# Kernel optimization log

Measured on AMD Instinct MI355X. Metric: run time of the kernel, lower is better.

The kernel has to match this reference:

```python
import jax, jax.numpy as jnp
import numpy as np

BATCH, SEQ, D_MODEL, D_STATE = 8, 4096, 128, 128


def setup_inputs() -> dict:
    key = jax.random.key(0)
    ks = jax.random.split(key, 6)
    x = jax.random.normal(ks[0], (BATCH, SEQ, D_MODEL), jnp.float32)
    # Stable (negative) eigenvalues so A_discrete = exp(dt*Lambda) < 1 and powers don't overflow.
    Lam = -(jax.random.uniform(ks[1], (D_STATE,), jnp.float32) * 2.0 + 0.1)
    B = jax.random.normal(ks[2], (D_STATE, D_MODEL), jnp.float32) / np.sqrt(D_STATE)
    C = jax.random.normal(ks[3], (D_MODEL, D_STATE), jnp.float32) / np.sqrt(D_STATE)
    Dv = jax.random.normal(ks[4], (D_MODEL,), jnp.float32)
    log_dt = (jax.random.uniform(ks[5], (D_MODEL,), jnp.float32)
              * (np.log(0.001) - np.log(0.1)) + np.log(0.1)).astype(jnp.float32)
    return {"x": x, "Lam": Lam, "B": B, "C": C, "Dv": Dv, "log_dt": log_dt}


def _s4_forward(x, Lam, B, C, Dv, log_dt):
    # x: (batch, L, M) with transposed=False
    _, L, M = x.shape
    dt = jnp.exp(log_dt)                                    # (M,)
    rate = dt[:, None] * Lam[None, :]                       # (M, N) = log(A_discrete)
    ell = jnp.arange(L, dtype=x.dtype)                      # (L,)
    # powers[m, s, l] = A_discrete[m, s] ** l  (closed form of the sequential cumprod)
    powers = jnp.exp(rate[:, :, None] * ell[None, None, :])  # (M, N, L)
    # Original: einsum('ds,msl->dsl', B, powers) sums over m, giving B[d,s]*Psum[s,l];
    # then einsum('md,dsl->ml', C, .) contracts d and s -> kernel = C @ B @ Psum.
    Psum = powers.sum(axis=0)                               # (N, L)
    kernel = C @ (B @ Psum)                                 # (M, L)
    xt = jnp.transpose(x, (0, 2, 1))                        # (B, M, L)
    n = 2 * L  # zero-padded linear convolution via FFT
    y_fft = jnp.fft.rfft(xt, n=n) * jnp.fft.rfft(kernel, n=n)[None]
    y = jnp.fft.irfft(y_fft, n=n)[..., :L]                  # (B, M, L)
    y = y + Dv[None, :, None] * xt                          # skip connection D*u
    return jnp.transpose(y, (0, 2, 1))                      # (B, L, M)


def reference(x, Lam, B, C, Dv, log_dt):
    return _s4_forward(x, Lam, B, C, Dv, log_dt)
```

## Files before the change

kernel.cpp:

```cpp
#include <hip/hip_runtime.h>
#include <math.h>

#define BATCH 8
#define SEQ   4096
#define DM    128
#define DS    128
#define N2    4096
#define NT    256
#define NTP   256

__device__ __forceinline__ float2 cmulf(float2 a, float2 b) {
    return make_float2(a.x * b.x - a.y * b.y, a.x * b.y + a.y * b.x);
}
__device__ __forceinline__ float2 caddf(float2 a, float2 b) { return make_float2(a.x + b.x, a.y + b.y); }
__device__ __forceinline__ float2 csubf(float2 a, float2 b) { return make_float2(a.x - b.x, a.y - b.y); }
__device__ __forceinline__ float2 conjf2(float2 a) { return make_float2(a.x, -a.y); }
__device__ __forceinline__ float2 cisf(float t) { float s, c; __sincosf(t, &s, &c); return make_float2(c, s); }

__device__ __forceinline__ int nibrev(int k) { return ((k & 15) << 8) | (k & 0xF0) | (k >> 8); }
__device__ __forceinline__ int physi(int a) { return a ^ ((a >> 4) & 15); }

__device__ __forceinline__ void dft16_fwd(const float2 x[16], float2 Xh[16]) {
    const float2 W[10] = { {1.f,0.f},
        {0.92387953f,-0.38268343f},{0.70710678f,-0.70710678f},{0.38268343f,-0.92387953f},
        {0.f,-1.f},{-0.38268343f,-0.92387953f},{-0.70710678f,-0.70710678f},
        {-0.92387953f,-0.38268343f},{-1.f,0.f},{-0.92387953f,0.38268343f} };
    float2 y[16];
#pragma unroll
    for (int j = 0; j < 4; ++j) {
        float2 a0 = x[j], a1 = x[j+4], a2 = x[j+8], a3 = x[j+12];
        float2 t0 = caddf(a0,a2), t1 = csubf(a0,a2);
        float2 t2 = caddf(a1,a3), t3 = csubf(a1,a3);
        float2 b1 = make_float2(t1.x + t3.y, t1.y - t3.x);
        float2 b3 = make_float2(t1.x - t3.y, t1.y + t3.x);
        y[j]    = caddf(t0,t2);
        y[j+4]  = cmulf(b1, W[j]);
        y[j+8]  = cmulf(csubf(t0,t2), W[2*j]);
        y[j+12] = cmulf(b3, W[3*j]);
    }
#pragma unroll
    for (int g = 0; g < 4; ++g) {
        float2 a0 = y[4*g], a1 = y[4*g+1], a2 = y[4*g+2], a3 = y[4*g+3];
        float2 t0 = caddf(a0,a2), t1 = csubf(a0,a2);
        float2 t2 = caddf(a1,a3), t3 = csubf(a1,a3);
        Xh[4*g]   = caddf(t0,t2);
        Xh[4*g+1] = make_float2(t1.x + t3.y, t1.y - t3.x);
        Xh[4*g+2] = csubf(t0,t2);
        Xh[4*g+3] = make_float2(t1.x - t3.y, t1.y + t3.x);
    }
}
__device__ __forceinline__ void dft16_inv(const float2 x[16], float2 Xh[16]) {
    const float2 W[10] = { {1.f,0.f},
        {0.92387953f,0.38268343f},{0.70710678f,0.70710678f},{0.38268343f,0.92387953f},
        {0.f,1.f},{-0.38268343f,0.92387953f},{-0.70710678f,0.70710678f},
        {-0.92387953f,0.38268343f},{-1.f,0.f},{-0.92387953f,-0.38268343f} };
    float2 y[16];
#pragma unroll
    for (int j = 0; j < 4; ++j) {
        float2 a0 = x[j], a1 = x[j+4], a2 = x[j+8], a3 = x[j+12];
        float2 t0 = caddf(a0,a2), t1 = csubf(a0,a2);
        float2 t2 = caddf(a1,a3), t3 = csubf(a1,a3);
        float2 b1 = make_float2(t1.x - t3.y, t1.y + t3.x);
        float2 b3 = make_float2(t1.x + t3.y, t1.y - t3.x);
        y[j]    = caddf(t0,t2);
        y[j+4]  = cmulf(b1, W[j]);
        y[j+8]  = cmulf(csubf(t0,t2), W[2*j]);
        y[j+12] = cmulf(b3, W[3*j]);
    }
#pragma unroll
    for (int g = 0; g < 4; ++g) {
        float2 a0 = y[4*g], a1 = y[4*g+1], a2 = y[4*g+2], a3 = y[4*g+3];
        float2 t0 = caddf(a0,a2), t1 = csubf(a0,a2);
        float2 t2 = caddf(a1,a3), t3 = csubf(a1,a3);
        Xh[4*g]   = caddf(t0,t2);
        Xh[4*g+1] = make_float2(t1.x - t3.y, t1.y + t3.x);
        Xh[4*g+2] = csubf(t0,t2);
        Xh[4*g+3] = make_float2(t1.x + t3.y, t1.y - t3.x);
    }
}


template<int Q>
__device__ __forceinline__ void stage_fwd(float2* z, int t) {
    float2 x[16], Xh[16];
    int adr[16];
    if (Q == 16) {
        int j = t & 15, top = t >> 4;
#pragma unroll
        for (int r = 0; r < 16; ++r) adr[r] = (top << 8) + (r << 4) + (j ^ r);
    } else {
        int j4 = t & 15;
#pragma unroll
        for (int r = 0; r < 16; ++r) adr[r] = (t << 4) + (j4 ^ r);
    }
#pragma unroll
    for (int r = 0; r < 16; ++r) x[r] = z[adr[r]];
    dft16_fwd(x, Xh);
    if (Q > 1) {
        int j = t & (Q - 1);
        float2 w1 = cisf(-(float)M_PI / (8.0f * (float)Q) * (float)j);
        float2 w = make_float2(1.f, 0.f);
#pragma unroll
        for (int k = 0; k < 16; ++k) {
            int sk = ((k & 3) << 2) | (k >> 2);
            z[adr[k]] = cmulf(Xh[sk], w);
            w = cmulf(w, w1);
        }
    } else {
#pragma unroll
        for (int k = 0; k < 16; ++k) {
            int sk = ((k & 3) << 2) | (k >> 2);
            z[adr[k]] = Xh[sk];
        }
    }
}

template<int Q>
__device__ __forceinline__ void stage_inv(float2* z, int t) {
    float2 x[16], Xh[16];
    int adr[16];
    if (Q == 16) {
        int j = t & 15, top = t >> 4;
#pragma unroll
        for (int r = 0; r < 16; ++r) adr[r] = (top << 8) + (r << 4) + (j ^ r);
    } else {
        int j4 = t & 15;
#pragma unroll
        for (int r = 0; r < 16; ++r) adr[r] = (t << 4) + (j4 ^ r);
    }
    if (Q > 1) {
        int j = t & (Q - 1);
        float2 w1 = cisf((float)M_PI / (8.0f * (float)Q) * (float)j);
        float2 w = make_float2(1.f, 0.f);
#pragma unroll
        for (int k = 0; k < 16; ++k) {
            x[k] = cmulf(z[adr[k]], w);
            w = cmulf(w, w1);
        }
    } else {
#pragma unroll
        for (int k = 0; k < 16; ++k) x[k] = z[adr[k]];
    }
    dft16_inv(x, Xh);
#pragma unroll
    for (int r = 0; r < 16; ++r) {
        int sr = ((r & 3) << 2) | (r >> 2);
        z[adr[r]] = Xh[sr];
    }
}

__device__ __forceinline__ void fwd_first(float2* z, const float2* __restrict__ vrow, int t) {
    float2 x[16], Xh[16];
#pragma unroll
    for (int r = 0; r < 8; ++r) x[r] = vrow[t + (r << 8)];
#pragma unroll
    for (int r = 8; r < 16; ++r) x[r] = make_float2(0.f, 0.f);
    dft16_fwd(x, Xh);
    int b0 = t ^ ((t >> 4) & 15);
    float2 w1 = cisf(-(float)M_PI / 2048.0f * (float)t);
    float2 w = make_float2(1.f, 0.f);
#pragma unroll
    for (int k = 0; k < 16; ++k) {
        int sk = ((k & 3) << 2) | (k >> 2);
        z[b0 + (k << 8)] = cmulf(Xh[sk], w);
        w = cmulf(w, w1);
    }
}

__device__ __forceinline__ void inv_last_store(const float2* z, float2* __restrict__ xrow,
                                               int t, float dv) {
    float2 x[16], Xh[16];
    int b0 = t ^ ((t >> 4) & 15);
    float2 w1 = cisf((float)M_PI / 2048.0f * (float)t);
    float2 w = make_float2(1.f, 0.f);
#pragma unroll
    for (int k = 0; k < 16; ++k) {
        x[k] = cmulf(z[b0 + (k << 8)], w);
        w = cmulf(w, w1);
    }
    dft16_inv(x, Xh);
    const float invN = 1.0f / 4096.0f;
#pragma unroll
    for (int r = 0; r < 8; ++r) {
        int sr = ((r & 3) << 2) | (r >> 2);
        float2 res = Xh[sr];
        float2 xv = xrow[t + (r << 8)];
        xrow[t + (r << 8)] = make_float2(res.x * invN + dv * xv.x, res.y * invN + dv * xv.y);
    }
}

__device__ __forceinline__ void pq_one(float2 Kk, float2 Kkp, float thk,
                                       float2 fap, float2 fbp,
                                       float2* P, float2* Q) {
    float2 e  = cisf(-thk);
    float2 fa = make_float2(0.5f * (1.f + e.y), -0.5f * e.x);
    float2 fb = make_float2(0.5f * (1.f - e.y),  0.5f * e.x);
    float2 ak = cmulf(Kk, fa), bk = cmulf(Kk, fb);
    float2 apv = cmulf(Kkp, fap), bpv = cmulf(Kkp, fbp);
    float2 g = make_float2(0.5f * (1.f + e.y), 0.5f * e.x);
    float2 h = make_float2(0.5f * (1.f - e.y), -0.5f * e.x);
    *P = caddf(cmulf(g, ak), cmulf(h, conjf2(bpv)));
    *Q = caddf(cmulf(g, bk), cmulf(h, conjf2(apv)));
}
__device__ __forceinline__ void pq_pair(float2 Kk, float2 Kkp, float thk, float thkp,
                                        float2* Pk, float2* Qk, float2* Pkp, float2* Qkp) {
    float2 e  = cisf(-thk);
    float2 ep = cisf(-thkp);
    float2 fa  = make_float2(0.5f * (1.f + e.y),  -0.5f * e.x);
    float2 fb  = make_float2(0.5f * (1.f - e.y),   0.5f * e.x);
    float2 fap = make_float2(0.5f * (1.f + ep.y), -0.5f * ep.x);
    float2 fbp = make_float2(0.5f * (1.f - ep.y),  0.5f * ep.x);
    pq_one(Kk,  Kkp, thk,  fap, fbp, Pk,  Qk);
    pq_one(Kkp, Kk,  thkp, fa,  fb,  Pkp, Qkp);
}


__global__ void prep_G(const float* __restrict__ Cm, const float* __restrict__ Bm,
                       float* __restrict__ GT) {
    int gid = blockIdx.x * blockDim.x + threadIdx.x;
    int m = gid >> 7, j = gid & 127;
    float acc = 0.f;
    for (int i = 0; i < DS; ++i) acc += Cm[m * DS + i] * Bm[i * DM + j];
    GT[j * DM + m] = acc;
}

__global__ void prep_psum2(const float* __restrict__ Lam, const float* __restrict__ logdt,
                           float* __restrict__ Psum) {
    __shared__ float E[DM];
    int s = blockIdx.x >> 1, half = blockIdx.x & 1;
    int t = threadIdx.x;
    if (t < DM) E[t] = __expf(logdt[t]) * Lam[s];
    __syncthreads();
    int l0 = t + 2048 * half;
    float acc[8] = {0.f,0.f,0.f,0.f,0.f,0.f,0.f,0.f};
    for (int m = 0; m < DM; ++m) {
        float e = E[m];
        float w = __expf(e * (float)l0);
        float r = __expf(e * 256.0f);
#pragma unroll
        for (int i = 0; i < 8; ++i) { acc[i] += w; w *= r; }
    }
#pragma unroll
    for (int i = 0; i < 8; ++i) Psum[s * SEQ + l0 + 256 * i] = acc[i];
}

__global__ void prep_K2(const float* __restrict__ GT, const float* __restrict__ Psum,
                        float* __restrict__ K) {
    __shared__ float4 PT[DS][4];
    int l0 = blockIdx.x * 16;
    int t = threadIdx.x;
    for (int idx = t; idx < 512; idx += NTP) {
        int s = idx >> 2, q = idx & 3;
        PT[s][q] = ((const float4*)(Psum + s * SEQ + l0))[q];
    }
    __syncthreads();
    int m = t & 127, half = t >> 7;
    float acc[8] = {0.f,0.f,0.f,0.f,0.f,0.f,0.f,0.f};
    for (int s = 0; s < DS; ++s) {
        float g = GT[s * DM + m];
        float4 p0 = PT[s][half * 2], p1 = PT[s][half * 2 + 1];
        acc[0] += g * p0.x; acc[1] += g * p0.y; acc[2] += g * p0.z; acc[3] += g * p0.w;
        acc[4] += g * p1.x; acc[5] += g * p1.y; acc[6] += g * p1.z; acc[7] += g * p1.w;
    }
    float4* kp = (float4*)(K + (size_t)m * SEQ + l0 + half * 8);
    kp[0] = make_float4(acc[0], acc[1], acc[2], acc[3]);
    kp[1] = make_float4(acc[4], acc[5], acc[6], acc[7]);
}

__global__ void __launch_bounds__(NT, 4) fftK_PQ(const float* __restrict__ K,
                                                 float4* __restrict__ PQ) {
    __shared__ __align__(16) float2 z[N2];
    int t = threadIdx.x, m = blockIdx.x;
    const float2* krow = (const float2*)(K + (size_t)m * SEQ);

    fwd_first(z, krow, t);  __syncthreads();
    stage_fwd<16>(z, t);    __syncthreads();
    stage_fwd<1>(z, t);     __syncthreads();

    float4* dst = PQ + (size_t)m * 4096;
#pragma unroll
    for (int c = 0; c < 8; ++c) {
        int idx2 = (((c << 8) | t)) << 1;
        int pos = (t << 4) | c;
        float2 Pk, Qk, Pkp, Qkp;
        if (pos == 0) {
            float2 v0 = z[0];
            float2 v2 = z[8];
            float2 Ku0    = make_float2(v0.x + v0.y, 0.f);
            float2 Ku4096 = make_float2(v0.x - v0.y, 0.f);
            float2 Ku2048 = conjf2(v2);
            float2 Pd, Qd;
            pq_pair(Ku0, Ku4096, 0.f, (float)M_PI, &Pk, &Qk, &Pd, &Qd);
            float th2 = 0.5f * (float)M_PI;
            pq_pair(Ku2048, Ku2048, th2, th2, &Pkp, &Qkp, &Pd, &Qd);
        } else {
            int k  = nibrev(pos);
            int kp = 4096 - k;
            float2 va = z[physi(pos)];
            float2 vb = z[physi(nibrev(kp))];
            float thk  = (float)M_PI * (float)k / 4096.0f;
            float thkp = (float)M_PI - thk;
            float2 e  = cisf(-thk);
            float2 cb = conjf2(vb);
            float2 s  = caddf(va, cb), d = csubf(va, cb);
            float2 pr = cmulf(e, d);
            float2 Kuk = make_float2(0.5f * (s.x + pr.y), 0.5f * (s.y - pr.x));
            float2 ep = make_float2(-e.x, e.y);
            float2 ca = conjf2(va);
            float2 s2 = caddf(vb, ca), d2 = csubf(vb, ca);
            float2 p2 = cmulf(ep, d2);
            float2 Kukp = make_float2(0.5f * (s2.x + p2.y), 0.5f * (s2.y - p2.x));
            pq_pair(Kuk, Kukp, thk, thkp, &Pk, &Qk, &Pkp, &Qkp);
        }
        dst[idx2]     = make_float4(Pk.x, Pk.y, Qk.x, Qk.y);
        dst[idx2 + 1] = make_float4(Pkp.x, Pkp.y, Qkp.x, Qkp.y);
    }
}

__global__ void __launch_bounds__(NT, 4) conv16(float* __restrict__ xt,
                                                const float4* __restrict__ PQ,
                                                const float* __restrict__ Dv) {
    __shared__ __align__(16) float2 z[N2];
    int t = threadIdx.x;
    int m = blockIdx.x & (DM - 1);
    int b = blockIdx.x >> 7;
    float2* xrow = (float2*)(xt + (((size_t)b * DM + m) << 12));

    fwd_first(z, xrow, t);  __syncthreads();
    stage_fwd<16>(z, t);    __syncthreads();
    stage_fwd<1>(z, t);     __syncthreads();

    {
        const float4* pq = PQ + (size_t)m * 4096;
#pragma unroll
        for (int c = 0; c < 8; ++c) {
            int idx2 = (((c << 8) | t)) << 1;
            int pos = (t << 4) | c;
            float4 lo = pq[idx2];
            float4 hi = pq[idx2 + 1];
            if (pos == 0) {
                float2 v0 = z[0];
                z[0] = caddf(cmulf(make_float2(lo.x, lo.y), v0),
                             cmulf(make_float2(lo.z, lo.w), conjf2(v0)));
                float2 v2 = z[8];
                z[8] = caddf(cmulf(make_float2(hi.x, hi.y), v2),
                             cmulf(make_float2(hi.z, hi.w), conjf2(v2)));
            } else {
                int k  = nibrev(pos);
                int i  = physi(pos);
                int ip = physi(nibrev(4096 - k));
                float2 va = z[i], vb = z[ip];
                z[i]  = caddf(cmulf(make_float2(lo.x, lo.y), va),
                              cmulf(make_float2(lo.z, lo.w), conjf2(vb)));
                z[ip] = caddf(cmulf(make_float2(hi.x, hi.y), vb),
                              cmulf(make_float2(hi.z, hi.w), conjf2(va)));
            }
        }
    }
    __syncthreads();

    stage_inv<1>(z, t);     __syncthreads();
    stage_inv<16>(z, t);    __syncthreads();
    inv_last_store(z, xrow, t, Dv[m]);
}

__global__ void transpose_xin(const float* __restrict__ x, float* __restrict__ xt) {
    __shared__ float tile[32][33];
    int b = blockIdx.z;
    int l0 = blockIdx.x * 32, m0 = blockIdx.y * 32;
    int t = threadIdx.x;
    int lr = t >> 3, mc4 = (t & 7) * 4;
    float4 v = *(const float4*)&x[(size_t)b * SEQ * DM + (size_t)(l0 + lr) * DM + m0 + mc4];
    tile[lr][mc4 + 0] = v.x; tile[lr][mc4 + 1] = v.y;
    tile[lr][mc4 + 2] = v.z; tile[lr][mc4 + 3] = v.w;
    __syncthreads();
    int mr = t >> 3, lc4 = (t & 7) * 4;
    float4 o = make_float4(tile[lc4 + 0][mr], tile[lc4 + 1][mr],
                           tile[lc4 + 2][mr], tile[lc4 + 3][mr]);
    *(float4*)&xt[(size_t)b * DM * SEQ + (size_t)(m0 + mr) * SEQ + l0 + lc4] = o;
}

__global__ void transpose_yout(const float* __restrict__ yt, float* __restrict__ out) {
    __shared__ float tile[32][33];
    int b = blockIdx.z;
    int l0 = blockIdx.x * 32, m0 = blockIdx.y * 32;
    int t = threadIdx.x;
    int mr = t >> 3, lc4 = (t & 7) * 4;
    float4 v = *(const float4*)&yt[(size_t)b * DM * SEQ + (size_t)(m0 + mr) * SEQ + l0 + lc4];
    tile[mr][lc4 + 0] = v.x; tile[mr][lc4 + 1] = v.y;
    tile[mr][lc4 + 2] = v.z; tile[mr][lc4 + 3] = v.w;
    __syncthreads();
    int lr = t >> 3, mc4 = (t & 7) * 4;
    float4 o = make_float4(tile[mc4 + 0][lr], tile[mc4 + 1][lr],
                           tile[mc4 + 2][lr], tile[mc4 + 3][lr]);
    *(float4*)&out[(size_t)b * SEQ * DM + (size_t)(l0 + lr) * DM + m0 + mc4] = o;
}

extern "C" void kernel_launch(void* const* d_in, const int* in_sizes, int n_in,
                              void* d_out, int out_size, void* d_ws, size_t ws_size,
                              hipStream_t stream) {
    const float* x     = (const float*)d_in[0];
    const float* Lam   = (const float*)d_in[1];
    const float* Bm    = (const float*)d_in[2];
    const float* Cm    = (const float*)d_in[3];
    const float* Dv    = (const float*)d_in[4];
    const float* logdt = (const float*)d_in[5];
    float* out = (float*)d_out;

    float*  ws   = (float*)d_ws;
    float*  xt   = ws;
    float4* PQ   = (float4*)(ws + 4194304);
    float*  K    = ws + 4194304 + 2097152;
    float*  Psum = K + 524288;
    float*  GT   = Psum + 524288;

    hipLaunchKernelGGL(prep_G,         dim3(64),         dim3(NTP),  0, stream, Cm, Bm, GT);
    hipLaunchKernelGGL(prep_psum2,     dim3(256),        dim3(NTP),  0, stream, Lam, logdt, Psum);
    hipLaunchKernelGGL(prep_K2,        dim3(256),        dim3(NTP),  0, stream, GT, Psum, K);
    hipLaunchKernelGGL(fftK_PQ,        dim3(128),        dim3(NT),   0, stream, K, PQ);
    hipLaunchKernelGGL(transpose_xin,  dim3(128, 4, 8),  dim3(NT),   0, stream, x, xt);
    hipLaunchKernelGGL(conv16,         dim3(1024),       dim3(NT),   0, stream, xt, PQ, Dv);
    hipLaunchKernelGGL(transpose_yout, dim3(128, 4, 8),  dim3(NT),   0, stream, xt, out);
}
```

Before: 134.8 us.

## Process two batch rows per FFT convolution block to reuse spectral filter loads

The convolution kernel now handles two batch elements for the same channel in one block, with two shared-memory FFT buffers. Each PQ filter coefficient load is shared across both rows, and per-thread twiddle computation and address setup are amortized over two independent FFTs, which also adds instruction-level parallelism. In exchange the grid halves to 512 blocks, shared memory per block doubles, register pressure roughly doubles, and launch bounds drop to 2 blocks per SM, which lowers occupancy.

```diff
diff --git a/kernel.cpp b/kernel.cpp
--- a/kernel.cpp
+++ b/kernel.cpp
@@ -115,40 +115,6 @@
     }
 }
 
-template<int Q>
-__device__ __forceinline__ void stage_inv(float2* z, int t) {
-    float2 x[16], Xh[16];
-    int adr[16];
-    if (Q == 16) {
-        int j = t & 15, top = t >> 4;
-#pragma unroll
-        for (int r = 0; r < 16; ++r) adr[r] = (top << 8) + (r << 4) + (j ^ r);
-    } else {
-        int j4 = t & 15;
-#pragma unroll
-        for (int r = 0; r < 16; ++r) adr[r] = (t << 4) + (j4 ^ r);
-    }
-    if (Q > 1) {
-        int j = t & (Q - 1);
-        float2 w1 = cisf((float)M_PI / (8.0f * (float)Q) * (float)j);
-        float2 w = make_float2(1.f, 0.f);
-#pragma unroll
-        for (int k = 0; k < 16; ++k) {
-            x[k] = cmulf(z[adr[k]], w);
-            w = cmulf(w, w1);
-        }
-    } else {
-#pragma unroll
-        for (int k = 0; k < 16; ++k) x[k] = z[adr[k]];
-    }
-    dft16_inv(x, Xh);
-#pragma unroll
-    for (int r = 0; r < 16; ++r) {
-        int sr = ((r & 3) << 2) | (r >> 2);
-        z[adr[r]] = Xh[sr];
-    }
-}
-
 __device__ __forceinline__ void fwd_first(float2* z, const float2* __restrict__ vrow, int t) {
     float2 x[16], Xh[16];
 #pragma unroll
@@ -167,25 +133,127 @@
     }
 }
 
-__device__ __forceinline__ void inv_last_store(const float2* z, float2* __restrict__ xrow,
-                                               int t, float dv) {
-    float2 x[16], Xh[16];
+
+template<int Q>
+__device__ __forceinline__ void stage_fwd2(float2* z0, float2* z1, int t) {
+    float2 x0[16], X0[16], x1[16], X1[16];
+    int adr[16];
+    if (Q == 16) {
+        int j = t & 15, top = t >> 4;
+#pragma unroll
+        for (int r = 0; r < 16; ++r) adr[r] = (top << 8) + (r << 4) + (j ^ r);
+    } else {
+        int j4 = t & 15;
+#pragma unroll
+        for (int r = 0; r < 16; ++r) adr[r] = (t << 4) + (j4 ^ r);
+    }
+#pragma unroll
+    for (int r = 0; r < 16; ++r) { x0[r] = z0[adr[r]]; x1[r] = z1[adr[r]]; }
+    dft16_fwd(x0, X0);
+    dft16_fwd(x1, X1);
+    if (Q > 1) {
+        int j = t & (Q - 1);
+        float2 w1 = cisf(-(float)M_PI / (8.0f * (float)Q) * (float)j);
+        float2 w = make_float2(1.f, 0.f);
+#pragma unroll
+        for (int k = 0; k < 16; ++k) {
+            int sk = ((k & 3) << 2) | (k >> 2);
+            z0[adr[k]] = cmulf(X0[sk], w);
+            z1[adr[k]] = cmulf(X1[sk], w);
+            w = cmulf(w, w1);
+        }
+    } else {
+#pragma unroll
+        for (int k = 0; k < 16; ++k) {
+            int sk = ((k & 3) << 2) | (k >> 2);
+            z0[adr[k]] = X0[sk];
+            z1[adr[k]] = X1[sk];
+        }
+    }
+}
+
+template<int Q>
+__device__ __forceinline__ void stage_inv2(float2* z0, float2* z1, int t) {
+    float2 x0[16], X0[16], x1[16], X1[16];
+    int adr[16];
+    if (Q == 16) {
+        int j = t & 15, top = t >> 4;
+#pragma unroll
+        for (int r = 0; r < 16; ++r) adr[r] = (top << 8) + (r << 4) + (j ^ r);
+    } else {
+        int j4 = t & 15;
+#pragma unroll
+        for (int r = 0; r < 16; ++r) adr[r] = (t << 4) + (j4 ^ r);
+    }
+    if (Q > 1) {
+        int j = t & (Q - 1);
+        float2 w1 = cisf((float)M_PI / (8.0f * (float)Q) * (float)j);
+        float2 w = make_float2(1.f, 0.f);
+#pragma unroll
+        for (int k = 0; k < 16; ++k) {
+            x0[k] = cmulf(z0[adr[k]], w);
+            x1[k] = cmulf(z1[adr[k]], w);
+            w = cmulf(w, w1);
+        }
+    } else {
+#pragma unroll
+        for (int k = 0; k < 16; ++k) { x0[k] = z0[adr[k]]; x1[k] = z1[adr[k]]; }
+    }
+    dft16_inv(x0, X0);
+    dft16_inv(x1, X1);
+#pragma unroll
+    for (int r = 0; r < 16; ++r) {
+        int sr = ((r & 3) << 2) | (r >> 2);
+        z0[adr[r]] = X0[sr];
+        z1[adr[r]] = X1[sr];
+    }
+}
+
+__device__ __forceinline__ void fwd_first2(float2* z0, float2* z1,
+                                           const float2* __restrict__ v0,
+                                           const float2* __restrict__ v1, int t) {
+    float2 x0[16], X0[16], x1[16], X1[16];
+#pragma unroll
+    for (int r = 0; r < 8; ++r) { x0[r] = v0[t + (r << 8)]; x1[r] = v1[t + (r << 8)]; }
+#pragma unroll
+    for (int r = 8; r < 16; ++r) { x0[r] = make_float2(0.f,0.f); x1[r] = make_float2(0.f,0.f); }
+    dft16_fwd(x0, X0);
+    dft16_fwd(x1, X1);
+    int b0 = t ^ ((t >> 4) & 15);
+    float2 w1 = cisf(-(float)M_PI / 2048.0f * (float)t);
+    float2 w = make_float2(1.f, 0.f);
+#pragma unroll
+    for (int k = 0; k < 16; ++k) {
+        int sk = ((k & 3) << 2) | (k >> 2);
+        z0[b0 + (k << 8)] = cmulf(X0[sk], w);
+        z1[b0 + (k << 8)] = cmulf(X1[sk], w);
+        w = cmulf(w, w1);
+    }
+}
+
+__device__ __forceinline__ void inv_last_store2(const float2* z0, const float2* z1,
+                                                float2* __restrict__ v0, float2* __restrict__ v1,
+                                                int t, float dv) {
+    float2 x0[16], X0[16], x1[16], X1[16];
     int b0 = t ^ ((t >> 4) & 15);
     float2 w1 = cisf((float)M_PI / 2048.0f * (float)t);
     float2 w = make_float2(1.f, 0.f);
 #pragma unroll
     for (int k = 0; k < 16; ++k) {
-        x[k] = cmulf(z[b0 + (k << 8)], w);
+        x0[k] = cmulf(z0[b0 + (k << 8)], w);
+        x1[k] = cmulf(z1[b0 + (k << 8)], w);
         w = cmulf(w, w1);
     }
-    dft16_inv(x, Xh);
+    dft16_inv(x0, X0);
+    dft16_inv(x1, X1);
     const float invN = 1.0f / 4096.0f;
 #pragma unroll
     for (int r = 0; r < 8; ++r) {
         int sr = ((r & 3) << 2) | (r >> 2);
-        float2 res = Xh[sr];
-        float2 xv = xrow[t + (r << 8)];
-        xrow[t + (r << 8)] = make_float2(res.x * invN + dv * xv.x, res.y * invN + dv * xv.y);
+        float2 xv0 = v0[t + (r << 8)];
+        float2 xv1 = v1[t + (r << 8)];
+        v0[t + (r << 8)] = make_float2(X0[sr].x * invN + dv * xv0.x, X0[sr].y * invN + dv * xv0.y);
+        v1[t + (r << 8)] = make_float2(X1[sr].x * invN + dv * xv1.x, X1[sr].y * invN + dv * xv1.y);
     }
 }
 
@@ -317,18 +385,20 @@
     }
 }
 
-__global__ void __launch_bounds__(NT, 4) conv16(float* __restrict__ xt,
-                                                const float4* __restrict__ PQ,
-                                                const float* __restrict__ Dv) {
-    __shared__ __align__(16) float2 z[N2];
+__global__ void __launch_bounds__(NT, 2) conv2(float* __restrict__ xt,
+                                               const float4* __restrict__ PQ,
+                                               const float* __restrict__ Dv) {
+    __shared__ __align__(16) float2 z0[N2];
+    __shared__ __align__(16) float2 z1[N2];
     int t = threadIdx.x;
-    int m = blockIdx.x & (DM - 1);
-    int b = blockIdx.x >> 7;
-    float2* xrow = (float2*)(xt + (((size_t)b * DM + m) << 12));
-
-    fwd_first(z, xrow, t);  __syncthreads();
-    stage_fwd<16>(z, t);    __syncthreads();
-    stage_fwd<1>(z, t);     __syncthreads();
+    int m  = blockIdx.x & (DM - 1);
+    int pr = blockIdx.x >> 7;
+    float2* xrow0 = (float2*)(xt + (((size_t)(2 * pr) * DM + m) << 12));
+    float2* xrow1 = (float2*)(xt + (((size_t)(2 * pr + 1) * DM + m) << 12));
+
+    fwd_first2(z0, z1, xrow0, xrow1, t);  __syncthreads();
+    stage_fwd2<16>(z0, z1, t);            __syncthreads();
+    stage_fwd2<1>(z0, z1, t);             __syncthreads();
 
     {
         const float4* pq = PQ + (size_t)m * 4096;
@@ -338,30 +408,33 @@
             int pos = (t << 4) | c;
             float4 lo = pq[idx2];
             float4 hi = pq[idx2 + 1];
+            float2 Plo = make_float2(lo.x, lo.y), Qlo = make_float2(lo.z, lo.w);
+            float2 Phi = make_float2(hi.x, hi.y), Qhi = make_float2(hi.z, hi.w);
             if (pos == 0) {
-                float2 v0 = z[0];
-                z[0] = caddf(cmulf(make_float2(lo.x, lo.y), v0),
-                             cmulf(make_float2(lo.z, lo.w), conjf2(v0)));
-                float2 v2 = z[8];
-                z[8] = caddf(cmulf(make_float2(hi.x, hi.y), v2),
-                             cmulf(make_float2(hi.z, hi.w), conjf2(v2)));
+                float2 a0 = z0[0], a1 = z1[0];
+                z0[0] = caddf(cmulf(Plo, a0), cmulf(Qlo, conjf2(a0)));
+                z1[0] = caddf(cmulf(Plo, a1), cmulf(Qlo, conjf2(a1)));
+                float2 b0 = z0[8], b1 = z1[8];
+                z0[8] = caddf(cmulf(Phi, b0), cmulf(Qhi, conjf2(b0)));
+                z1[8] = caddf(cmulf(Phi, b1), cmulf(Qhi, conjf2(b1)));
             } else {
                 int k  = nibrev(pos);
                 int i  = physi(pos);
                 int ip = physi(nibrev(4096 - k));
-                float2 va = z[i], vb = z[ip];
-                z[i]  = caddf(cmulf(make_float2(lo.x, lo.y), va),
-                              cmulf(make_float2(lo.z, lo.w), conjf2(vb)));
-                z[ip] = caddf(cmulf(make_float2(hi.x, hi.y), vb),
-                              cmulf(make_float2(hi.z, hi.w), conjf2(va)));
+                float2 va0 = z0[i], vb0 = z0[ip];
+                float2 va1 = z1[i], vb1 = z1[ip];
+                z0[i]  = caddf(cmulf(Plo, va0), cmulf(Qlo, conjf2(vb0)));
+                z0[ip] = caddf(cmulf(Phi, vb0), cmulf(Qhi, conjf2(va0)));
+                z1[i]  = caddf(cmulf(Plo, va1), cmulf(Qlo, conjf2(vb1)));
+                z1[ip] = caddf(cmulf(Phi, vb1), cmulf(Qhi, conjf2(va1)));
             }
         }
     }
     __syncthreads();
 
-    stage_inv<1>(z, t);     __syncthreads();
-    stage_inv<16>(z, t);    __syncthreads();
-    inv_last_store(z, xrow, t, Dv[m]);
+    stage_inv2<1>(z0, z1, t);             __syncthreads();
+    stage_inv2<16>(z0, z1, t);            __syncthreads();
+    inv_last_store2(z0, z1, xrow0, xrow1, t, Dv[m]);
 }
 
 __global__ void transpose_xin(const float* __restrict__ x, float* __restrict__ xt) {
@@ -419,6 +492,6 @@
     hipLaunchKernelGGL(prep_K2,        dim3(256),        dim3(NTP),  0, stream, GT, Psum, K);
     hipLaunchKernelGGL(fftK_PQ,        dim3(128),        dim3(NT),   0, stream, K, PQ);
     hipLaunchKernelGGL(transpose_xin,  dim3(128, 4, 8),  dim3(NT),   0, stream, x, xt);
-    hipLaunchKernelGGL(conv16,         dim3(1024),       dim3(NT),   0, stream, xt, PQ, Dv);
+    hipLaunchKernelGGL(conv2,          dim3(512),        dim3(NT),   0, stream, xt, PQ, Dv);
     hipLaunchKernelGGL(transpose_yout, dim3(128, 4, 8),  dim3(NT),   0, stream, xt, out);
 }
```

Result: no change. 136.8 us (+1.4%).

## Fuse spectral multiply into first inverse FFT stage and merge prep kernels

Applied to the files above, without the earlier changes.

The conv kernel now computes the pointwise spectral product into registers per thread and feeds it directly into a radix-16 inverse DFT. This replaces a separate shared-memory write pass, a barrier and the stage_inv<1> pass. The PQ coefficient table is re-laid out (pqslot) so each thread's 16 coefficients load with coalesced access. The prep_G and prep_psum kernels are merged into one launch to cut launch overhead. Each thread now reads 32 shared values with a less regular pattern for the partner index, and the fused block keeps more registers live.

```diff
diff --git a/kernel.cpp b/kernel.cpp
--- a/kernel.cpp
+++ b/kernel.cpp
@@ -19,6 +19,7 @@
 
 __device__ __forceinline__ int nibrev(int k) { return ((k & 15) << 8) | (k & 0xF0) | (k >> 8); }
 __device__ __forceinline__ int physi(int a) { return a ^ ((a >> 4) & 15); }
+__device__ __forceinline__ int pqslot(int p) { return ((p & 15) << 8) | (p >> 4); }
 
 __device__ __forceinline__ void dft16_fwd(const float2 x[16], float2 Xh[16]) {
     const float2 W[10] = { {1.f,0.f},
@@ -214,34 +215,33 @@
     pq_one(Kkp, Kk,  thkp, fa,  fb,  Pkp, Qkp);
 }
 
-
-__global__ void prep_G(const float* __restrict__ Cm, const float* __restrict__ Bm,
-                       float* __restrict__ GT) {
-    int gid = blockIdx.x * blockDim.x + threadIdx.x;
-    int m = gid >> 7, j = gid & 127;
-    float acc = 0.f;
-    for (int i = 0; i < DS; ++i) acc += Cm[m * DS + i] * Bm[i * DM + j];
-    GT[j * DM + m] = acc;
-}
-
-__global__ void prep_psum2(const float* __restrict__ Lam, const float* __restrict__ logdt,
-                           float* __restrict__ Psum) {
-    __shared__ float E[DM];
-    int s = blockIdx.x >> 1, half = blockIdx.x & 1;
-    int t = threadIdx.x;
-    if (t < DM) E[t] = __expf(logdt[t]) * Lam[s];
-    __syncthreads();
-    int l0 = t + 2048 * half;
-    float acc[8] = {0.f,0.f,0.f,0.f,0.f,0.f,0.f,0.f};
-    for (int m = 0; m < DM; ++m) {
-        float e = E[m];
-        float w = __expf(e * (float)l0);
-        float r = __expf(e * 256.0f);
-#pragma unroll
-        for (int i = 0; i < 8; ++i) { acc[i] += w; w *= r; }
-    }
-#pragma unroll
-    for (int i = 0; i < 8; ++i) Psum[s * SEQ + l0 + 256 * i] = acc[i];
+__global__ void __launch_bounds__(NTP) prep_GP(
+    const float* __restrict__ Lam, const float* __restrict__ logdt, float* __restrict__ Psum,
+    const float* __restrict__ Cm, const float* __restrict__ Bm, float* __restrict__ GT) {
+    int bid = blockIdx.x, t = threadIdx.x;
+    if (bid < 256) {
+        __shared__ float E[DM];
+        int s = bid >> 1, half = bid & 1;
+        if (t < DM) E[t] = __expf(logdt[t]) * Lam[s];
+        __syncthreads();
+        int l0 = t + 2048 * half;
+        float acc[8] = {0.f,0.f,0.f,0.f,0.f,0.f,0.f,0.f};
+        for (int m = 0; m < DM; ++m) {
+            float e = E[m];
+            float w = __expf(e * (float)l0);
+            float r = __expf(e * 256.0f);
+#pragma unroll
+            for (int i = 0; i < 8; ++i) { acc[i] += w; w *= r; }
+        }
+#pragma unroll
+        for (int i = 0; i < 8; ++i) Psum[s * SEQ + l0 + 256 * i] = acc[i];
+    } else {
+        int gid = (bid - 256) * NTP + t;
+        int m = gid >> 7, j = gid & 127;
+        float acc = 0.f;
+        for (int i = 0; i < DS; ++i) acc += Cm[m * DS + i] * Bm[i * DM + j];
+        GT[j * DM + m] = acc;
+    }
 }
 
 __global__ void prep_K2(const float* __restrict__ GT, const float* __restrict__ Psum,
@@ -280,7 +280,6 @@
     float4* dst = PQ + (size_t)m * 4096;
 #pragma unroll
     for (int c = 0; c < 8; ++c) {
-        int idx2 = (((c << 8) | t)) << 1;
         int pos = (t << 4) | c;
         float2 Pk, Qk, Pkp, Qkp;
         if (pos == 0) {
@@ -293,11 +292,14 @@
             pq_pair(Ku0, Ku4096, 0.f, (float)M_PI, &Pk, &Qk, &Pd, &Qd);
             float th2 = 0.5f * (float)M_PI;
             pq_pair(Ku2048, Ku2048, th2, th2, &Pkp, &Qkp, &Pd, &Qd);
+            dst[pqslot(0)] = make_float4(Pk.x, Pk.y, Qk.x, Qk.y);
+            dst[pqslot(8)] = make_float4(Pkp.x, Pkp.y, Qkp.x, Qkp.y);
         } else {
             int k  = nibrev(pos);
             int kp = 4096 - k;
+            int ppos = nibrev(kp);
             float2 va = z[physi(pos)];
-            float2 vb = z[physi(nibrev(kp))];
+            float2 vb = z[physi(ppos)];
             float thk  = (float)M_PI * (float)k / 4096.0f;
             float thkp = (float)M_PI - thk;
             float2 e  = cisf(-thk);
@@ -311,9 +313,9 @@
             float2 p2 = cmulf(ep, d2);
             float2 Kukp = make_float2(0.5f * (s2.x + p2.y), 0.5f * (s2.y - p2.x));
             pq_pair(Kuk, Kukp, thk, thkp, &Pk, &Qk, &Pkp, &Qkp);
-        }
-        dst[idx2]     = make_float4(Pk.x, Pk.y, Qk.x, Qk.y);
-        dst[idx2 + 1] = make_float4(Pkp.x, Pkp.y, Qkp.x, Qkp.y);
+            dst[pqslot(pos)]  = make_float4(Pk.x, Pk.y, Qk.x, Qk.y);
+            dst[pqslot(ppos)] = make_float4(Pkp.x, Pkp.y, Qkp.x, Qkp.y);
+        }
     }
 }
 
@@ -330,36 +332,35 @@
     stage_fwd<16>(z, t);    __syncthreads();
     stage_fwd<1>(z, t);     __syncthreads();
 
+    float2 x[16];
     {
         const float4* pq = PQ + (size_t)m * 4096;
-#pragma unroll
-        for (int c = 0; c < 8; ++c) {
-            int idx2 = (((c << 8) | t)) << 1;
-            int pos = (t << 4) | c;
-            float4 lo = pq[idx2];
-            float4 hi = pq[idx2 + 1];
-            if (pos == 0) {
-                float2 v0 = z[0];
-                z[0] = caddf(cmulf(make_float2(lo.x, lo.y), v0),
-                             cmulf(make_float2(lo.z, lo.w), conjf2(v0)));
-                float2 v2 = z[8];
-                z[8] = caddf(cmulf(make_float2(hi.x, hi.y), v2),
-                             cmulf(make_float2(hi.z, hi.w), conjf2(v2)));
-            } else {
-                int k  = nibrev(pos);
-                int i  = physi(pos);
-                int ip = physi(nibrev(4096 - k));
-                float2 va = z[i], vb = z[ip];
-                z[i]  = caddf(cmulf(make_float2(lo.x, lo.y), va),
-                              cmulf(make_float2(lo.z, lo.w), conjf2(vb)));
-                z[ip] = caddf(cmulf(make_float2(hi.x, hi.y), vb),
-                              cmulf(make_float2(hi.z, hi.w), conjf2(va)));
-            }
+        int j4 = t & 15;
+#pragma unroll
+        for (int r = 0; r < 16; ++r) {
+            int pos = (t << 4) | r;
+            float2 va = z[(t << 4) + (r ^ j4)];
+            int k  = nibrev(pos);
+            int kp = (4096 - k) & 4095;
+            float2 vb = z[physi(nibrev(kp))];
+            float4 co = pq[(r << 8) | t];
+            x[r] = caddf(cmulf(make_float2(co.x, co.y), va),
+                         cmulf(make_float2(co.z, co.w), conjf2(vb)));
         }
     }
     __syncthreads();
-
-    stage_inv<1>(z, t);     __syncthreads();
+    {
+        float2 Xh[16];
+        dft16_inv(x, Xh);
+        int j4 = t & 15;
+#pragma unroll
+        for (int r = 0; r < 16; ++r) {
+            int sr = ((r & 3) << 2) | (r >> 2);
+            z[(t << 4) + (r ^ j4)] = Xh[sr];
+        }
+    }
+    __syncthreads();
+
     stage_inv<16>(z, t);    __syncthreads();
     inv_last_store(z, xrow, t, Dv[m]);
 }
@@ -414,8 +415,8 @@
     float*  Psum = K + 524288;
     float*  GT   = Psum + 524288;
 
-    hipLaunchKernelGGL(prep_G,         dim3(64),         dim3(NTP),  0, stream, Cm, Bm, GT);
-    hipLaunchKernelGGL(prep_psum2,     dim3(256),        dim3(NTP),  0, stream, Lam, logdt, Psum);
+    hipLaunchKernelGGL(prep_GP,        dim3(320),        dim3(NTP),  0, stream,
+                       Lam, logdt, Psum, Cm, Bm, GT);
     hipLaunchKernelGGL(prep_K2,        dim3(256),        dim3(NTP),  0, stream, GT, Psum, K);
     hipLaunchKernelGGL(fftK_PQ,        dim3(128),        dim3(NT),   0, stream, K, PQ);
     hipLaunchKernelGGL(transpose_xin,  dim3(128, 4, 8),  dim3(NT),   0, stream, x, xt);
```

Measured after the change: 131.7 us. 1.02x faster.
